# Kernel tuning notes

Hardware: AMD Instinct MI355X
Metric: run time of the kernel (lower is better)

The kernel has to match this reference:

```python
import jax, jax.numpy as jnp
import numpy as np

DISCOUNT = 0.99
LAMBD = 0.95


def setup_inputs() -> dict:
    key = jax.random.key(0)
    k1, k2 = jax.random.split(key)
    T, B = 1000, 32768
    rewards = jax.random.normal(k1, (T, B), dtype=jnp.float32)
    values = jax.random.normal(k2, (T, B), dtype=jnp.float32)
    masks = jnp.ones((T, B), dtype=jnp.float32)
    return {"rewards": rewards, "values": values, "masks": masks}


def reference(rewards, values, masks):
    # delta_t = r_t + gamma * m_t * (1 - lambda) * V_t
    delta = rewards + DISCOUNT * masks * (1.0 - LAMBD) * values
    gl = DISCOUNT * LAMBD

    def step(carry, inp):
        d_t, m_t = inp
        ret_t = d_t + carry * gl * m_t
        return ret_t, ret_t

    # reverse-time scan, initial carry is V_{T-1}
    _, returns = jax.lax.scan(step, values[-1], (delta, masks), reverse=True)
    return returns
```

## Files before the change

### kernel.cpp

```cpp
#include <hip/hip_runtime.h>


#define T_DIM 1000
#define B_DIM 32768

__global__ __launch_bounds__(64) void LambdaReturn_kernel(
    const float* __restrict__ rewards,
    const float* __restrict__ values,
    const float* __restrict__ masks,
    float* __restrict__ out) {
  const int b = blockIdx.x * blockDim.x + threadIdx.x;
  const float c_delta = 0.99f * (1.0f - 0.95f);
  const float gl      = 0.99f * 0.95f;

  float carry = values[(size_t)(T_DIM - 1) * B_DIM + b];

  #pragma unroll 8
  for (int t = T_DIM - 1; t >= 0; --t) {
    const size_t idx = (size_t)t * B_DIM + b;
    const float r = rewards[idx];
    const float v = values[idx];
    const float m = masks[idx];
    const float d = fmaf(c_delta * m, v, r);
    carry = fmaf(gl * m, carry, d);
    out[idx] = carry;
  }
}

extern "C" void kernel_launch(void* const* d_in, const int* in_sizes, int n_in,
                              void* d_out, int out_size, void* d_ws, size_t ws_size,
                              hipStream_t stream) {
  const float* rewards = (const float*)d_in[0];
  const float* values  = (const float*)d_in[1];
  const float* masks   = (const float*)d_in[2];
  float* out = (float*)d_out;

  dim3 grid(B_DIM / 64);
  dim3 block(64);
  LambdaReturn_kernel<<<grid, block, 0, stream>>>(rewards, values, masks, out);
}
```

Baseline: 412.1 us.

## Double-buffer timestep loads in register groups with nontemporal loads and stores

Splits the reverse time scan into groups of 20 timesteps and keeps two register buffers. The loads for the next group are issued while the current group is being computed, so more memory requests are in flight per thread on this latency-bound, low-occupancy scan. Loads and stores also use nontemporal hints to avoid polluting the cache with streaming data. The trade-off is higher register pressure from 120 buffered floats per thread.

New measurement: 365.1 us. 11.4% less time.

```diff
diff --git a/kernel.cpp b/kernel.cpp
--- a/kernel.cpp
+++ b/kernel.cpp
@@ -3,6 +3,8 @@
 
 #define T_DIM 1000
 #define B_DIM 32768
+#define U 20
+#define NGROUPS 50
 
 __global__ __launch_bounds__(64) void LambdaReturn_kernel(
     const float* __restrict__ rewards,
@@ -13,18 +15,47 @@
   const float c_delta = 0.99f * (1.0f - 0.95f);
   const float gl      = 0.99f * 0.95f;
 
-  float carry = values[(size_t)(T_DIM - 1) * B_DIM + b];
+  const float* pr = rewards + b;
+  const float* pv = values + b;
+  const float* pm = masks + b;
+  float* po = out + b;
 
-  #pragma unroll 8
-  for (int t = T_DIM - 1; t >= 0; --t) {
-    const size_t idx = (size_t)t * B_DIM + b;
-    const float r = rewards[idx];
-    const float v = values[idx];
-    const float m = masks[idx];
-    const float d = fmaf(c_delta * m, v, r);
-    carry = fmaf(gl * m, carry, d);
-    out[idx] = carry;
+  float carry = pv[(size_t)(T_DIM - 1) * B_DIM];
+
+  float rA[U], vA[U], mA[U];
+  float rB[U], vB[U], mB[U];
+
+  auto ld = [&](float* r, float* v, float* m, int g) {
+    const size_t base = (size_t)(T_DIM - 1 - U * g) * B_DIM;
+    #pragma unroll
+    for (int j = 0; j < U; ++j) {
+      const size_t idx = base - (size_t)j * B_DIM;
+      r[j] = __builtin_nontemporal_load(pr + idx);
+      v[j] = __builtin_nontemporal_load(pv + idx);
+      m[j] = __builtin_nontemporal_load(pm + idx);
+    }
+  };
+  auto cmp = [&](const float* r, const float* v, const float* m, int g) {
+    const size_t base = (size_t)(T_DIM - 1 - U * g) * B_DIM;
+    #pragma unroll
+    for (int j = 0; j < U; ++j) {
+      const float d = fmaf(c_delta * m[j], v[j], r[j]);
+      carry = fmaf(gl * m[j], carry, d);
+      __builtin_nontemporal_store(carry, po + (base - (size_t)j * B_DIM));
+    }
+  };
+
+  ld(rA, vA, mA, 0);
+  ld(rB, vB, mB, 1);
+
+  for (int g = 0; g < NGROUPS - 2; g += 2) {
+    cmp(rA, vA, mA, g);
+    ld(rA, vA, mA, g + 2);
+    cmp(rB, vB, mB, g + 1);
+    if (g + 3 < NGROUPS) ld(rB, vB, mB, g + 3);
   }
+  cmp(rA, vA, mA, NGROUPS - 2);
+  cmp(rB, vB, mB, NGROUPS - 1);
 }
 
 extern "C" void kernel_launch(void* const* d_in, const int* in_sizes, int n_in,
```
